# Kernel optimization log

Hardware: AMD Instinct MI355X
Metric: run time of the kernel (lower is better)

## Reference

```python
import jax, jax.numpy as jnp
import numpy as np

B, S, D, H = 4, 2048, 768, 12


def setup_inputs() -> dict:
    key = jax.random.key(0)
    k1, k2, k3, k4 = jax.random.split(key, 4)
    std = D ** (-0.5)
    x = jax.random.normal(k1, (B, S, D), dtype=jnp.float32)
    W_QKV = jax.random.normal(k2, (3, D, D), dtype=jnp.float32) * std
    W_O = jax.random.normal(k3, (D, D), dtype=jnp.float32) * std
    token_positions = jnp.sort(jax.random.randint(k4, (B, S), 0, S), axis=-1).astype(jnp.int64)
    return {"x": x, "W_QKV": W_QKV, "W_O": W_O, "token_positions": token_positions,
            "num_heads": H, "theta": 10000}


def _apply_rope(t, cos, sin):
    # t: (B, H, S, Hd); cos/sin: (B, 1, S, Hd/2). Interleaved even/odd pairs.
    te, to = t[..., 0::2], t[..., 1::2]
    re = te * cos - to * sin
    ro = te * sin + to * cos
    return jnp.stack([re, ro], axis=-1).reshape(t.shape)


def reference(x, W_QKV, W_O, token_positions, num_heads, theta):
    b, s, d = x.shape
    hd = d // num_heads  # d_head = d_k = d_v
    # fused QKV projection: Q = x @ W_QKV[0].T etc.
    qkv = jnp.einsum('bsd,kod->kbso', x, W_QKV)              # (3, B, S, D)
    qkv = qkv.reshape(3, b, s, num_heads, hd).transpose(0, 1, 3, 2, 4)  # (3, B, H, S, Hd)
    q, k, v = qkv[0], qkv[1], qkv[2]
    # RoPE angles: pos * theta^(-2j/d_k)
    inv_freq = jnp.asarray(theta, x.dtype) ** (-(jnp.arange(0, hd, 2, dtype=x.dtype) / hd))
    angles = token_positions.astype(x.dtype)[..., None] * inv_freq    # (B, S, Hd/2)
    cos = jnp.cos(angles)[:, None]                                     # (B, 1, S, Hd/2)
    sin = jnp.sin(angles)[:, None]
    q = _apply_rope(q, cos, sin)
    k = _apply_rope(k, cos, sin)
    # causal attention
    scores = jnp.einsum('bhqd,bhkd->bhqk', q, k) / (hd ** 0.5)        # (B, H, S, S)
    causal = jnp.tril(jnp.ones((s, s), dtype=bool))
    scores = jnp.where(causal, scores, -jnp.inf)
    probs = jax.nn.softmax(scores, axis=-1)
    out = jnp.einsum('bhqk,bhkd->bhqd', probs, v)                      # (B, H, S, Hd)
    out = out.transpose(0, 2, 1, 3).reshape(b, s, d)
    return out @ W_O.T
```

## Files before the change

kernel.cpp:

```cpp
#include <hip/hip_runtime.h>
#include <hip/hip_bf16.h>

typedef __bf16 bf16;
typedef __bf16 bf16x8 __attribute__((ext_vector_type(8)));
typedef __bf16 bf16x4 __attribute__((ext_vector_type(4)));
typedef short  s16x4  __attribute__((ext_vector_type(4)));
typedef float  f32x4  __attribute__((ext_vector_type(4)));

#if defined(__has_builtin)
#if __has_builtin(__builtin_amdgcn_mfma_f32_16x16x16bf16_1k)
#define HAVE_MFMA16 1
#endif
#if __has_builtin(__builtin_amdgcn_exp2f)
#define EXP2(x) __builtin_amdgcn_exp2f(x)
#else
#define EXP2(x) exp2f(x)
#endif
#else
#define EXP2(x) exp2f(x)
#endif

__device__ __forceinline__ void gl_lds16(const void* g, void* l) {
  __builtin_amdgcn_global_load_lds(
      (__attribute__((address_space(1))) const void*)g,
      (__attribute__((address_space(3))) void*)l, 16, 0, 0);
}

__device__ __forceinline__ f32x4 mfma32(bf16x8 a, bf16x8 b, f32x4 c) {
  return __builtin_amdgcn_mfma_f32_16x16x32_bf16(a, b, c, 0, 0, 0);
}
#if HAVE_MFMA16
__device__ __forceinline__ f32x4 mfma16(s16x4 a, s16x4 b, f32x4 c) {
  return __builtin_amdgcn_mfma_f32_16x16x16bf16_1k(a, b, c, 0, 0, 0);
}
#endif

__global__ void cvt3(const float* __restrict__ a, bf16* __restrict__ da,
                     const float* __restrict__ b, bf16* __restrict__ db,
                     const float* __restrict__ c, bf16* __restrict__ dc) {
  int bx = blockIdx.x;
  const float* s; bf16* d; int i;
  if (bx < 6144)      { s = a; d = da; i = bx * 256 + threadIdx.x; }
  else if (bx < 7872) { s = b; d = db; i = (bx - 6144) * 256 + threadIdx.x; }
  else                { s = c; d = dc; i = (bx - 7872) * 256 + threadIdx.x; }
  float4 v = ((const float4*)s)[i];
  bf16x4 o;
  o[0] = (bf16)v.x; o[1] = (bf16)v.y; o[2] = (bf16)v.z; o[3] = (bf16)v.w;
  ((bf16x4*)d)[i] = o;
}

template <int MODE>
__global__ void gemm_bt(const bf16* __restrict__ A, const bf16* __restrict__ Bm,
                        void* __restrict__ Cout, bf16* __restrict__ Vout) {
  constexpr int K = 768;
  __shared__ __align__(16) char As[2][128 * 64];
  __shared__ __align__(16) char Bs[2][128 * 64];
  const int tid = threadIdx.x;
  const int w = tid >> 6, lane = tid & 63;
  const int quad = lane >> 4, l15 = lane & 15;
  const int wrow = w >> 1, wcol = w & 1;
  const int m0 = blockIdx.x * 128, n0 = blockIdx.y * 128;

  f32x4 acc[4][4];
#pragma unroll
  for (int mt = 0; mt < 4; ++mt)
#pragma unroll
    for (int nt = 0; nt < 4; ++nt) acc[mt][nt] = (f32x4){0.f, 0.f, 0.f, 0.f};

  auto stage = [&](int k0, int bufi) {
#pragma unroll
    for (int i = 0; i < 2; ++i) {
      int L = i * 256 + tid;
      int r = L >> 2, cl = L & 3;
      int cg = cl ^ ((r >> 1) & 3);
      gl_lds16(A + (size_t)(m0 + r) * K + k0 + cg * 8, As[bufi] + (i * 256 + w * 64) * 16);
      gl_lds16(Bm + (size_t)(n0 + r) * K + k0 + cg * 8, Bs[bufi] + (i * 256 + w * 64) * 16);
    }
  };

  stage(0, 0);
  int buf = 0;

  for (int k0 = 0; k0 < K; k0 += 32) {
    __syncthreads();
    if (k0 + 32 < K) stage(k0 + 32, buf ^ 1);
    const char* Ab = As[buf];
    const char* Bb = Bs[buf];

    bf16x8 af[4], bfr[4];
#pragma unroll
    for (int mt = 0; mt < 4; ++mt) {
      int r = wrow * 64 + mt * 16 + l15;
      int cl = quad ^ ((r >> 1) & 3);
      af[mt] = *(const bf16x8*)(Ab + r * 64 + cl * 16);
    }
#pragma unroll
    for (int nt = 0; nt < 4; ++nt) {
      int r = wcol * 64 + nt * 16 + l15;
      int cl = quad ^ ((r >> 1) & 3);
      bfr[nt] = *(const bf16x8*)(Bb + r * 64 + cl * 16);
    }
#pragma unroll
    for (int mt = 0; mt < 4; ++mt)
#pragma unroll
      for (int nt = 0; nt < 4; ++nt)
        acc[mt][nt] = mfma32(af[mt], bfr[nt], acc[mt][nt]);
    buf ^= 1;
  }

#pragma unroll
  for (int mt = 0; mt < 4; ++mt)
#pragma unroll
    for (int nt = 0; nt < 4; ++nt)
#pragma unroll
      for (int r = 0; r < 4; ++r) {
        int m = m0 + wrow * 64 + mt * 16 + quad * 4 + r;
        int n = n0 + wcol * 64 + nt * 16 + l15;
        float v = acc[mt][nt][r];
        if (MODE == 0) {
          ((float*)Cout)[(size_t)m * 768 + n] = v;
        } else {
          int mat = n / 768, rem = n % 768;
          int hh = rem >> 6, d = rem & 63;
          int bb = m >> 11, s = m & 2047;
          if (mat == 2)
            Vout[(((size_t)(bb * 12 + hh) * 64 + d) * 2048) + s] = (bf16)v;
          else
            ((bf16*)Cout)[(((size_t)(mat * 4 + bb) * 12 + hh) * 2048 + s) * 64 + d] = (bf16)v;
        }
      }
}

__global__ void rope_k(bf16* __restrict__ qk, const int* __restrict__ tpos,
                       const int* __restrict__ thetap) {
  int i = blockIdx.x * 256 + threadIdx.x;
  int d2 = i & 31;
  int s = (i >> 5) & 2047;
  int rest = i >> 16;
  int rb = rest / 12;
  int b = rb & 3;
  size_t off = ((size_t)rest * 2048 + s) * 64 + d2 * 2;
  int pos = tpos[b * 2048 + s];
  float lt = log2f((float)(*thetap));
  float fr = exp2f(-(float)d2 * (1.0f / 32.0f) * lt);
  float ang = (float)pos * fr;
  float sn, cs;
  sincosf(ang, &sn, &cs);
  float scq = (rest < 48) ? 0.18033688011112042f : 1.0f;
  float te = (float)qk[off], to = (float)qk[off + 1];
  qk[off]     = (bf16)((te * cs - to * sn) * scq);
  qk[off + 1] = (bf16)((te * sn + to * cs) * scq);
}

__global__ __launch_bounds__(128, 3)
void attn(const bf16* __restrict__ qkv, const bf16* __restrict__ vt,
          bf16* __restrict__ aout) {
  const int bx = blockIdx.x;
  const int qt = 31 - (bx / 48);
  const int bh = bx % 48;
  const int b = bh / 12, h = bh % 12;
  const int tid = threadIdx.x, w = tid >> 6, lane = tid & 63;
  const int quad = lane >> 4, l15 = lane & 15;
  const bf16* Q  = qkv + (size_t)bh * (2048 * 64);
  const bf16* Kp = qkv + (size_t)(48 + bh) * (2048 * 64);
  const bf16* Vt = vt + (size_t)bh * (64 * 2048);
  __shared__ __align__(16) char Ks[2][64 * 128];
  __shared__ __align__(16) char Vs[2][64 * 128];

  const int qbase = qt * 64 + w * 32;
  bf16x8 qf[2][2];
#pragma unroll
  for (int j = 0; j < 2; ++j) {
    qf[j][0] = *(const bf16x8*)(Q + (size_t)(qbase + j * 16 + l15) * 64 + quad * 8);
    qf[j][1] = *(const bf16x8*)(Q + (size_t)(qbase + j * 16 + l15) * 64 + 32 + quad * 8);
  }

  float li[2] = {0.f, 0.f};
  f32x4 o[2][4];
#pragma unroll
  for (int j = 0; j < 2; ++j)
#pragma unroll
    for (int dt = 0; dt < 4; ++dt) o[j][dt] = (f32x4){0.f, 0.f, 0.f, 0.f};

  auto stage = [&](int kb, int bufi) {
#pragma unroll
    for (int i = 0; i < 4; ++i) {
      int L = i * 128 + tid;
      int r = L >> 3, cl = L & 7, cg = cl ^ (r & 7);
      gl_lds16(Kp + (size_t)(kb * 64 + r) * 64 + cg * 8, Ks[bufi] + L * 16);
      gl_lds16(Vt + (size_t)r * 2048 + kb * 64 + cg * 8, Vs[bufi] + L * 16);
    }
  };

  stage(0, 0);
  int buf = 0;

  for (int kb = 0; kb <= qt; ++kb) {
    __syncthreads();
    if (kb < qt) stage(kb + 1, buf ^ 1);
    const char* Kb = Ks[buf];
    const char* Vb = Vs[buf];

    float S[2][16];
#pragma unroll
    for (int sk = 0; sk < 4; ++sk) {
      int r = sk * 16 + l15;
      int cl0 = quad ^ (r & 7);
      int cl1 = (4 + quad) ^ (r & 7);
      bf16x8 kf0 = *(const bf16x8*)(Kb + r * 128 + cl0 * 16);
      bf16x8 kf1 = *(const bf16x8*)(Kb + r * 128 + cl1 * 16);
#pragma unroll
      for (int j = 0; j < 2; ++j) {
        f32x4 st = (f32x4){0.f, 0.f, 0.f, 0.f};
        st = mfma32(kf0, qf[j][0], st);
        st = mfma32(kf1, qf[j][1], st);
#pragma unroll
        for (int rr = 0; rr < 4; ++rr) S[j][sk * 4 + rr] = st[rr];
      }
    }
    if (kb == qt) {
#pragma unroll
      for (int j = 0; j < 2; ++j)
#pragma unroll
        for (int sk = 0; sk < 4; ++sk)
#pragma unroll
          for (int rr = 0; rr < 4; ++rr) {
            int key = kb * 64 + sk * 16 + quad * 4 + rr;
            if (key > qbase + j * 16 + l15) S[j][sk * 4 + rr] = -1e30f;
          }
    }

#if HAVE_MFMA16
    s16x4 pf[2][4];
#endif
#pragma unroll
    for (int j = 0; j < 2; ++j) {
      float rs = 0.f;
#pragma unroll
      for (int sk = 0; sk < 4; ++sk) {
        bf16x4 pb;
#pragma unroll
        for (int rr = 0; rr < 4; ++rr) {
          float p = EXP2(S[j][sk * 4 + rr]);
          rs += p;
          pb[rr] = (bf16)p;
#if !HAVE_MFMA16
          S[j][sk * 4 + rr] = p;
#endif
        }
#if HAVE_MFMA16
        pf[j][sk] = __builtin_bit_cast(s16x4, pb);
#else
        (void)pb;
#endif
      }
      rs += __shfl_xor(rs, 16);
      rs += __shfl_xor(rs, 32);
      li[j] += rs;
    }

#if HAVE_MFMA16
#pragma unroll
    for (int sk = 0; sk < 4; ++sk)
#pragma unroll
      for (int dt = 0; dt < 4; ++dt) {
        int rr = dt * 16 + l15;
        int c = sk * 2 + (quad >> 1);
        int cl = c ^ (rr & 7);
        s16x4 vf = *(const s16x4*)(Vb + rr * 128 + cl * 16 + (quad & 1) * 8);
        o[0][dt] = mfma16(pf[0][sk], vf, o[0][dt]);
        o[1][dt] = mfma16(pf[1][sk], vf, o[1][dt]);
      }
#else
#pragma unroll
    for (int j = 0; j < 2; ++j)
#pragma unroll
      for (int kc = 0; kc < 2; ++kc) {
        bf16x8 af;
#pragma unroll
        for (int jj = 0; jj < 8; ++jj) {
          int sq = (quad & 1) * 2 + (jj >> 2);
          int src = sq * 16 + l15;
          float v0 = __shfl(S[j][kc * 8 + (jj & 3)], src);
          float v1 = __shfl(S[j][kc * 8 + 4 + (jj & 3)], src);
          af[jj] = (bf16)((quad < 2) ? v0 : v1);
        }
#pragma unroll
        for (int dt = 0; dt < 4; ++dt) {
          int rr = dt * 16 + l15;
          int c = kc * 4 + quad;
          int cl = c ^ (rr & 7);
          bf16x8 vf = *(const bf16x8*)(Vb + rr * 128 + cl * 16);
          o[j][dt] = mfma32(af, vf, o[j][dt]);
        }
      }
#endif
    buf ^= 1;
  }

#pragma unroll
  for (int j = 0; j < 2; ++j) {
    float lr[4];
#pragma unroll
    for (int rr = 0; rr < 4; ++rr)
      lr[rr] = __builtin_amdgcn_rcpf(__shfl(li[j], quad * 4 + rr));
#pragma unroll
    for (int dt = 0; dt < 4; ++dt)
#pragma unroll
      for (int rr = 0; rr < 4; ++rr) {
        int q = qbase + j * 16 + quad * 4 + rr;
        int n = h * 64 + dt * 16 + l15;
        aout[((size_t)b * 2048 + q) * 768 + n] = (bf16)(o[j][dt][rr] * lr[rr]);
      }
  }
}

extern "C" void kernel_launch(void* const* d_in, const int* in_sizes, int n_in,
                              void* d_out, int out_size, void* d_ws, size_t ws_size,
                              hipStream_t stream) {
  const float* x    = (const float*)d_in[0];
  const float* wqkv = (const float*)d_in[1];
  const float* wo   = (const float*)d_in[2];
  const int* tpos   = (const int*)d_in[3];
  const int* thetap = (const int*)d_in[5];

  char* ws = (char*)d_ws;
  bf16* xb    = (bf16*)(ws);
  bf16* wqkvb = (bf16*)(ws + 12582912);
  bf16* wob   = (bf16*)(ws + 16121856);
  bf16* qkv   = (bf16*)(ws + 17301504);
  bf16* vtb   = (bf16*)(ws + 55050240);

  cvt3<<<8448, 256, 0, stream>>>(x, xb, wqkv, wqkvb, wo, wob);
  gemm_bt<1><<<dim3(64, 18), 256, 0, stream>>>(xb, wqkvb, (void*)qkv, vtb);
  rope_k<<<24576, 256, 0, stream>>>(qkv, tpos, thetap);
  attn<<<1536, 128, 0, stream>>>(qkv, vtb, xb);
  gemm_bt<0><<<dim3(64, 6), 256, 0, stream>>>(xb, wob, (void*)d_out, nullptr);
}
```

Before: 226.2 us.

## Fuse RoPE into QKV GEMM epilogue and enlarge attention blocks to 128 queries

Precomputes a cos/sin table for RoPE inside the conversion kernel and applies rotation plus query scaling in the QKV GEMM epilogue via a lane shuffle, which removes the separate rope kernel and its read-modify-write pass over Q and K. The attention kernel now uses 4 waves covering 128 queries per block, so each staged K/V tile is shared by twice as many waves and half as many blocks are launched. Waves skip tiles beyond their causal limit, and s_setprio is raised around the MFMA sections. The risks are idle waves during the extra tiles, the epilogue shuffle relying on adjacent-lane pairing, and lower occupancy tuning.

```diff
diff --git a/kernel.cpp b/kernel.cpp
--- a/kernel.cpp
+++ b/kernel.cpp
@@ -35,10 +35,24 @@
 }
 #endif
 
-__global__ void cvt3(const float* __restrict__ a, bf16* __restrict__ da,
+__global__ void prep(const float* __restrict__ a, bf16* __restrict__ da,
                      const float* __restrict__ b, bf16* __restrict__ db,
-                     const float* __restrict__ c, bf16* __restrict__ dc) {
+                     const float* __restrict__ c, bf16* __restrict__ dc,
+                     const int* __restrict__ tpos, const int* __restrict__ thetap,
+                     float2* __restrict__ tab) {
   int bx = blockIdx.x;
+  if (bx >= 8448) {
+    int i = (bx - 8448) * 256 + threadIdx.x;
+    int d2 = i & 31;
+    int bs = i >> 5;
+    float lt = log2f((float)(*thetap));
+    float fr = exp2f(-(float)d2 * (1.0f / 32.0f) * lt);
+    float ang = (float)tpos[bs] * fr;
+    float sn, cs;
+    sincosf(ang, &sn, &cs);
+    tab[i] = make_float2(cs, sn);
+    return;
+  }
   const float* s; bf16* d; int i;
   if (bx < 6144)      { s = a; d = da; i = bx * 256 + threadIdx.x; }
   else if (bx < 7872) { s = b; d = db; i = (bx - 6144) * 256 + threadIdx.x; }
@@ -51,7 +65,8 @@
 
 template <int MODE>
 __global__ void gemm_bt(const bf16* __restrict__ A, const bf16* __restrict__ Bm,
-                        void* __restrict__ Cout, bf16* __restrict__ Vout) {
+                        void* __restrict__ Cout, bf16* __restrict__ Vout,
+                        const float2* __restrict__ tab) {
   constexpr int K = 768;
   __shared__ __align__(16) char As[2][128 * 64];
   __shared__ __align__(16) char Bs[2][128 * 64];
@@ -123,40 +138,24 @@
           int mat = n / 768, rem = n % 768;
           int hh = rem >> 6, d = rem & 63;
           int bb = m >> 11, s = m & 2047;
-          if (mat == 2)
+          if (mat == 2) {
             Vout[(((size_t)(bb * 12 + hh) * 64 + d) * 2048) + s] = (bf16)v;
-          else
-            ((bf16*)Cout)[(((size_t)(mat * 4 + bb) * 12 + hh) * 2048 + s) * 64 + d] = (bf16)v;
-        }
-      }
-}
-
-__global__ void rope_k(bf16* __restrict__ qk, const int* __restrict__ tpos,
-                       const int* __restrict__ thetap) {
-  int i = blockIdx.x * 256 + threadIdx.x;
-  int d2 = i & 31;
-  int s = (i >> 5) & 2047;
-  int rest = i >> 16;
-  int rb = rest / 12;
-  int b = rb & 3;
-  size_t off = ((size_t)rest * 2048 + s) * 64 + d2 * 2;
-  int pos = tpos[b * 2048 + s];
-  float lt = log2f((float)(*thetap));
-  float fr = exp2f(-(float)d2 * (1.0f / 32.0f) * lt);
-  float ang = (float)pos * fr;
-  float sn, cs;
-  sincosf(ang, &sn, &cs);
-  float scq = (rest < 48) ? 0.18033688011112042f : 1.0f;
-  float te = (float)qk[off], to = (float)qk[off + 1];
-  qk[off]     = (bf16)((te * cs - to * sn) * scq);
-  qk[off + 1] = (bf16)((te * sn + to * cs) * scq);
-}
-
-__global__ __launch_bounds__(128, 3)
+          } else {
+            float partner = __shfl_xor(v, 1);
+            float2 t = tab[((size_t)m << 5) + ((rem >> 1) & 31)];
+            float out = v * t.x + ((n & 1) ? partner : -partner) * t.y;
+            if (mat == 0) out *= 0.18033688011112042f;
+            ((bf16*)Cout)[(((size_t)(mat * 4 + bb) * 12 + hh) * 2048 + s) * 64 + d] = (bf16)out;
+          }
+        }
+      }
+}
+
+__global__ __launch_bounds__(256, 4)
 void attn(const bf16* __restrict__ qkv, const bf16* __restrict__ vt,
           bf16* __restrict__ aout) {
   const int bx = blockIdx.x;
-  const int qt = 31 - (bx / 48);
+  const int qt = 15 - (bx / 48);
   const int bh = bx % 48;
   const int b = bh / 12, h = bh % 12;
   const int tid = threadIdx.x, w = tid >> 6, lane = tid & 63;
@@ -167,7 +166,8 @@
   __shared__ __align__(16) char Ks[2][64 * 128];
   __shared__ __align__(16) char Vs[2][64 * 128];
 
-  const int qbase = qt * 64 + w * 32;
+  const int qbase = qt * 128 + w * 32;
+  const int kmax = qbase >> 6;
   bf16x8 qf[2][2];
 #pragma unroll
   for (int j = 0; j < 2; ++j) {
@@ -184,8 +184,8 @@
 
   auto stage = [&](int kb, int bufi) {
 #pragma unroll
-    for (int i = 0; i < 4; ++i) {
-      int L = i * 128 + tid;
+    for (int i = 0; i < 2; ++i) {
+      int L = i * 256 + tid;
       int r = L >> 3, cl = L & 7, cg = cl ^ (r & 7);
       gl_lds16(Kp + (size_t)(kb * 64 + r) * 64 + cg * 8, Ks[bufi] + L * 16);
       gl_lds16(Vt + (size_t)r * 2048 + kb * 64 + cg * 8, Vs[bufi] + L * 16);
@@ -194,107 +194,114 @@
 
   stage(0, 0);
   int buf = 0;
-
-  for (int kb = 0; kb <= qt; ++kb) {
+  const int nkt = 2 * qt + 2;
+
+  for (int kb = 0; kb < nkt; ++kb) {
     __syncthreads();
-    if (kb < qt) stage(kb + 1, buf ^ 1);
-    const char* Kb = Ks[buf];
-    const char* Vb = Vs[buf];
-
-    float S[2][16];
-#pragma unroll
-    for (int sk = 0; sk < 4; ++sk) {
-      int r = sk * 16 + l15;
-      int cl0 = quad ^ (r & 7);
-      int cl1 = (4 + quad) ^ (r & 7);
-      bf16x8 kf0 = *(const bf16x8*)(Kb + r * 128 + cl0 * 16);
-      bf16x8 kf1 = *(const bf16x8*)(Kb + r * 128 + cl1 * 16);
+    if (kb + 1 < nkt) stage(kb + 1, buf ^ 1);
+    if (kb <= kmax) {
+      const char* Kb = Ks[buf];
+      const char* Vb = Vs[buf];
+
+      float S[2][16];
+      __builtin_amdgcn_s_setprio(1);
+#pragma unroll
+      for (int sk = 0; sk < 4; ++sk) {
+        int r = sk * 16 + l15;
+        int cl0 = quad ^ (r & 7);
+        int cl1 = (4 + quad) ^ (r & 7);
+        bf16x8 kf0 = *(const bf16x8*)(Kb + r * 128 + cl0 * 16);
+        bf16x8 kf1 = *(const bf16x8*)(Kb + r * 128 + cl1 * 16);
+#pragma unroll
+        for (int j = 0; j < 2; ++j) {
+          f32x4 st = (f32x4){0.f, 0.f, 0.f, 0.f};
+          st = mfma32(kf0, qf[j][0], st);
+          st = mfma32(kf1, qf[j][1], st);
+#pragma unroll
+          for (int rr = 0; rr < 4; ++rr) S[j][sk * 4 + rr] = st[rr];
+        }
+      }
+      __builtin_amdgcn_s_setprio(0);
+      if (kb == kmax) {
+#pragma unroll
+        for (int j = 0; j < 2; ++j)
+#pragma unroll
+          for (int sk = 0; sk < 4; ++sk)
+#pragma unroll
+            for (int rr = 0; rr < 4; ++rr) {
+              int key = kb * 64 + sk * 16 + quad * 4 + rr;
+              if (key > qbase + j * 16 + l15) S[j][sk * 4 + rr] = -1e30f;
+            }
+      }
+
+#if HAVE_MFMA16
+      s16x4 pf[2][4];
+#endif
 #pragma unroll
       for (int j = 0; j < 2; ++j) {
-        f32x4 st = (f32x4){0.f, 0.f, 0.f, 0.f};
-        st = mfma32(kf0, qf[j][0], st);
-        st = mfma32(kf1, qf[j][1], st);
-#pragma unroll
-        for (int rr = 0; rr < 4; ++rr) S[j][sk * 4 + rr] = st[rr];
-      }
-    }
-    if (kb == qt) {
-#pragma unroll
-      for (int j = 0; j < 2; ++j)
-#pragma unroll
-        for (int sk = 0; sk < 4; ++sk)
+        float rs = 0.f;
+#pragma unroll
+        for (int sk = 0; sk < 4; ++sk) {
+          bf16x4 pb;
 #pragma unroll
           for (int rr = 0; rr < 4; ++rr) {
-            int key = kb * 64 + sk * 16 + quad * 4 + rr;
-            if (key > qbase + j * 16 + l15) S[j][sk * 4 + rr] = -1e30f;
+            float p = EXP2(S[j][sk * 4 + rr]);
+            rs += p;
+            pb[rr] = (bf16)p;
+#if !HAVE_MFMA16
+            S[j][sk * 4 + rr] = p;
+#endif
           }
-    }
-
 #if HAVE_MFMA16
-    s16x4 pf[2][4];
-#endif
-#pragma unroll
-    for (int j = 0; j < 2; ++j) {
-      float rs = 0.f;
-#pragma unroll
-      for (int sk = 0; sk < 4; ++sk) {
-        bf16x4 pb;
-#pragma unroll
-        for (int rr = 0; rr < 4; ++rr) {
-          float p = EXP2(S[j][sk * 4 + rr]);
-          rs += p;
-          pb[rr] = (bf16)p;
-#if !HAVE_MFMA16
-          S[j][sk * 4 + rr] = p;
-#endif
-        }
+          pf[j][sk] = __builtin_bit_cast(s16x4, pb);
+#else
+          (void)pb;
+#endif
+        }
+        rs += __shfl_xor(rs, 16);
+        rs += __shfl_xor(rs, 32);
+        li[j] += rs;
+      }
+
 #if HAVE_MFMA16
-        pf[j][sk] = __builtin_bit_cast(s16x4, pb);
-#else
-        (void)pb;
-#endif
-      }
-      rs += __shfl_xor(rs, 16);
-      rs += __shfl_xor(rs, 32);
-      li[j] += rs;
-    }
-
-#if HAVE_MFMA16
-#pragma unroll
-    for (int sk = 0; sk < 4; ++sk)
-#pragma unroll
-      for (int dt = 0; dt < 4; ++dt) {
-        int rr = dt * 16 + l15;
-        int c = sk * 2 + (quad >> 1);
-        int cl = c ^ (rr & 7);
-        s16x4 vf = *(const s16x4*)(Vb + rr * 128 + cl * 16 + (quad & 1) * 8);
-        o[0][dt] = mfma16(pf[0][sk], vf, o[0][dt]);
-        o[1][dt] = mfma16(pf[1][sk], vf, o[1][dt]);
-      }
-#else
-#pragma unroll
-    for (int j = 0; j < 2; ++j)
-#pragma unroll
-      for (int kc = 0; kc < 2; ++kc) {
-        bf16x8 af;
-#pragma unroll
-        for (int jj = 0; jj < 8; ++jj) {
-          int sq = (quad & 1) * 2 + (jj >> 2);
-          int src = sq * 16 + l15;
-          float v0 = __shfl(S[j][kc * 8 + (jj & 3)], src);
-          float v1 = __shfl(S[j][kc * 8 + 4 + (jj & 3)], src);
-          af[jj] = (bf16)((quad < 2) ? v0 : v1);
-        }
+      __builtin_amdgcn_s_setprio(1);
+#pragma unroll
+      for (int sk = 0; sk < 4; ++sk)
 #pragma unroll
         for (int dt = 0; dt < 4; ++dt) {
           int rr = dt * 16 + l15;
-          int c = kc * 4 + quad;
+          int c = sk * 2 + (quad >> 1);
           int cl = c ^ (rr & 7);
-          bf16x8 vf = *(const bf16x8*)(Vb + rr * 128 + cl * 16);
-          o[j][dt] = mfma32(af, vf, o[j][dt]);
-        }
-      }
-#endif
+          s16x4 vf = *(const s16x4*)(Vb + rr * 128 + cl * 16 + (quad & 1) * 8);
+          o[0][dt] = mfma16(pf[0][sk], vf, o[0][dt]);
+          o[1][dt] = mfma16(pf[1][sk], vf, o[1][dt]);
+        }
+      __builtin_amdgcn_s_setprio(0);
+#else
+#pragma unroll
+      for (int j = 0; j < 2; ++j)
+#pragma unroll
+        for (int kc = 0; kc < 2; ++kc) {
+          bf16x8 af;
+#pragma unroll
+          for (int jj = 0; jj < 8; ++jj) {
+            int sq = (quad & 1) * 2 + (jj >> 2);
+            int src = sq * 16 + l15;
+            float v0 = __shfl(S[j][kc * 8 + (jj & 3)], src);
+            float v1 = __shfl(S[j][kc * 8 + 4 + (jj & 3)], src);
+            af[jj] = (bf16)((quad < 2) ? v0 : v1);
+          }
+#pragma unroll
+          for (int dt = 0; dt < 4; ++dt) {
+            int rr = dt * 16 + l15;
+            int c = kc * 4 + quad;
+            int cl = c ^ (rr & 7);
+            bf16x8 vf = *(const bf16x8*)(Vb + rr * 128 + cl * 16);
+            o[j][dt] = mfma32(af, vf, o[j][dt]);
+          }
+        }
+#endif
+    }
     buf ^= 1;
   }
 
@@ -330,10 +337,10 @@
   bf16* wob   = (bf16*)(ws + 16121856);
   bf16* qkv   = (bf16*)(ws + 17301504);
   bf16* vtb   = (bf16*)(ws + 55050240);
-
-  cvt3<<<8448, 256, 0, stream>>>(x, xb, wqkv, wqkvb, wo, wob);
-  gemm_bt<1><<<dim3(64, 18), 256, 0, stream>>>(xb, wqkvb, (void*)qkv, vtb);
-  rope_k<<<24576, 256, 0, stream>>>(qkv, tpos, thetap);
-  attn<<<1536, 128, 0, stream>>>(qkv, vtb, xb);
-  gemm_bt<0><<<dim3(64, 6), 256, 0, stream>>>(xb, wob, (void*)d_out, nullptr);
-}
+  float2* tab = (float2*)(ws + 42467328);
+
+  prep<<<9472, 256, 0, stream>>>(x, xb, wqkv, wqkvb, wo, wob, tpos, thetap, tab);
+  gemm_bt<1><<<dim3(64, 18), 256, 0, stream>>>(xb, wqkvb, (void*)qkv, vtb, tab);
+  attn<<<768, 256, 0, stream>>>(qkv, vtb, xb);
+  gemm_bt<0><<<dim3(64, 6), 256, 0, stream>>>(xb, wob, (void*)d_out, nullptr, nullptr);
+}
```

New measurement: 228.8 us. About the same (+1.1%).
